# Performance work log

Measured on AMD Instinct MI355X. Metric: run time of the kernel, lower is better.

Reference implementation:

```python
import jax, jax.numpy as jnp
import numpy as np

B, C, W, H = 4, 256, 64, 64
D = C // 8  # reduced query/key channels


def setup_inputs() -> dict:
    key = jax.random.key(0)
    k1, k2, k3, k4, k5 = jax.random.split(key, 5)
    return {
        "x": jax.random.normal(k1, (B, C, W, H), dtype=jnp.float32),
        "q_weight": jax.random.normal(k2, (D, C), dtype=jnp.float32) * 0.05,
        "k_weight": jax.random.normal(k3, (D, C), dtype=jnp.float32) * 0.05,
        "v_weight": jax.random.normal(k4, (C, C), dtype=jnp.float32) * 0.05,
        "gamma": jax.random.normal(k5, (1,), dtype=jnp.float32),
    }


def reference(x, q_weight, k_weight, v_weight, gamma):
    b, c, w, h = x.shape
    n = w * h
    xf = x.reshape(b, c, n)                       # (B, C, N)
    # 1x1 convs == channel matmuls
    q = jnp.einsum('dc,bcn->bdn', q_weight, xf)   # (B, D, N)
    k = jnp.einsum('dc,bcn->bdn', k_weight, xf)   # (B, D, N)
    v = jnp.einsum('oc,bcn->bon', v_weight, xf)   # (B, C, N)
    # energy[b, i, j] = <q[:, i], k[:, j]>  (unscaled, single head)
    energy = jnp.einsum('bdi,bdj->bij', q, k)     # (B, N, N)
    attn = jax.nn.softmax(energy, axis=-1)        # softmax over keys j
    # out[b, c, i] = sum_j v[b, c, j] * attn[b, i, j]
    out = jnp.einsum('bcj,bij->bci', v, attn)     # (B, C, N)
    out = out.reshape(b, c, w, h)
    return gamma[0] * out + x
```

## Files before the change

kernel.cpp:

```cpp
#include <hip/hip_runtime.h>
#include <math.h>

#define Bb 4
#define Cc 256
#define Nn 4096
#define Dd 32
#define XST 264

typedef __attribute__((ext_vector_type(8))) short bf16x8;
typedef __attribute__((ext_vector_type(4))) float f32x4;

__device__ __forceinline__ unsigned short f2bf(float x) {
    union { float f; unsigned u; } c; c.f = x;
    unsigned r = c.u + 0x7fffu + ((c.u >> 16) & 1u);
    return (unsigned short)(r >> 16);
}
__device__ __forceinline__ unsigned pk2(float a, float b) {
    return (unsigned)f2bf(a) | ((unsigned)f2bf(b) << 16);
}
__device__ __forceinline__ float fexp2(float x) {
#if __has_builtin(__builtin_amdgcn_exp2f)
    return __builtin_amdgcn_exp2f(x);
#else
    return __exp2f(x);
#endif
}
__device__ __forceinline__ void wg_barrier() {
    asm volatile("s_waitcnt lgkmcnt(0)\n\ts_barrier" ::: "memory");
}
template <int CTRL>
__device__ __forceinline__ float dppf(float v) {
    int iv = __builtin_bit_cast(int, v);
    return __builtin_bit_cast(float,
        __builtin_amdgcn_update_dpp(iv, iv, CTRL, 0xF, 0xF, false));
}
__device__ __forceinline__ float rowsum16(float v) {
    v += dppf<0xB1>(v);
    v += dppf<0x4E>(v);
    v += dppf<0x141>(v);
    v += dppf<0x140>(v);
    return v;
}

__global__ __launch_bounds__(256) void pack_w(
    const float* __restrict__ qw, const float* __restrict__ kw,
    const float* __restrict__ vw, short* __restrict__ wpk) {
    const int g = blockIdx.x * 256 + threadIdx.x;
    const int qd = g & 3, m = (g >> 2) & 15, kc = (g >> 6) & 7, ot = g >> 9;
    const int o = 16 * ot + m;
    const float* src;
    float scale = 1.0f;
    if (o < 32)      { src = qw + (size_t)o * Cc; scale = 1.44269504088896f; }
    else if (o < 64) { src = kw + (size_t)(o - 32) * Cc; }
    else             { src = vw + (size_t)(o - 64) * Cc; }
    const float* s8 = src + 32 * kc + 8 * qd;
    uint4 u;
    u.x = pk2(s8[0] * scale, s8[1] * scale);
    u.y = pk2(s8[2] * scale, s8[3] * scale);
    u.z = pk2(s8[4] * scale, s8[5] * scale);
    u.w = pk2(s8[6] * scale, s8[7] * scale);
    *(uint4*)(wpk + (size_t)g * 8) = u;
}

__global__ __launch_bounds__(256) void proj(
    const float* __restrict__ x, const short* __restrict__ wpk,
    short* __restrict__ q_t, short* __restrict__ k_t, short* __restrict__ v_b) {
    __shared__ alignas(16) short xs[32 * XST];
    __shared__ alignas(16) short vstage[16384];
    const int b = blockIdx.z;
    const int jt = blockIdx.x;
    const int tid = threadIdx.x;
    const int w = tid >> 6;
    const int lane = tid & 63, qd = lane >> 4, m = lane & 15;

    for (int half = 0; half < 2; ++half) {
        const int n0 = jt * 64 + half * 32;
        if (half) __syncthreads();

        {
            const int n = tid & 31, cg = tid >> 5;
            const float* xp = x + ((size_t)b * Cc + 32 * cg) * Nn + n0 + n;
            float xv[32];
#pragma unroll
            for (int i = 0; i < 32; ++i) xv[i] = xp[(size_t)i * Nn];
            short* row = xs + n * XST + 32 * cg;
#pragma unroll
            for (int u4 = 0; u4 < 4; ++u4)
                *(uint4*)(row + 8 * u4) = make_uint4(
                    pk2(xv[8*u4+0], xv[8*u4+1]), pk2(xv[8*u4+2], xv[8*u4+3]),
                    pk2(xv[8*u4+4], xv[8*u4+5]), pk2(xv[8*u4+6], xv[8*u4+7]));
        }
        __syncthreads();

        const int fslot = m * 4 + qd;
        f32x4 acc[5][2];
#pragma unroll
        for (int i = 0; i < 5; ++i)
#pragma unroll
            for (int nt = 0; nt < 2; ++nt) acc[i][nt] = (f32x4){0.f, 0.f, 0.f, 0.f};

        bf16x8 afc[5], afn[5];
#pragma unroll
        for (int i = 0; i < 5; ++i)
            afc[i] = *(const bf16x8*)(wpk + ((size_t)((4*i + w) * 8 + 0) * 64 + fslot) * 8);

        for (int kc = 0; kc < 8; ++kc) {
            if (kc < 7) {
#pragma unroll
                for (int i = 0; i < 5; ++i)
                    afn[i] = *(const bf16x8*)(
                        wpk + ((size_t)((4*i + w) * 8 + kc + 1) * 64 + fslot) * 8);
            }
            const bf16x8 b0 = *(const bf16x8*)&xs[(     m) * XST + 32 * kc + 8 * qd];
            const bf16x8 b1 = *(const bf16x8*)&xs[(16 + m) * XST + 32 * kc + 8 * qd];
#pragma unroll
            for (int i = 0; i < 5; ++i)
                acc[i][0] = __builtin_amdgcn_mfma_f32_16x16x32_bf16(afc[i], b0, acc[i][0], 0, 0, 0);
#pragma unroll
            for (int i = 0; i < 5; ++i)
                acc[i][1] = __builtin_amdgcn_mfma_f32_16x16x32_bf16(afc[i], b1, acc[i][1], 0, 0, 0);
#pragma unroll
            for (int i = 0; i < 5; ++i) afc[i] = afn[i];
        }

#pragma unroll
        for (int i = 0; i < 5; ++i) {
            const int ot = 4 * i + w;
            if (ot < 4) {
                short* dst = (ot < 2 ? q_t : k_t) + (size_t)b * Nn * Dd;
                const int dbase = (ot & 1) * 16 + 4 * qd;
#pragma unroll
                for (int nt = 0; nt < 2; ++nt) {
                    const f32x4 a = acc[i][nt];
                    *(uint2*)(dst + (size_t)(n0 + 16 * nt + m) * Dd + dbase) =
                        make_uint2(pk2(a[0], a[1]), pk2(a[2], a[3]));
                }
            } else {
                const int ct = ot - 4;
                const int b5 = half;
                const int vbase =
                    ((ct * 2 + (m >> 3)) * 64 + ((m >> 1) & 3) * 16 + 4 * qd) * 8
                    + 4 * (m & 1) + 2 * b5;
#pragma unroll
                for (int rr = 0; rr < 4; ++rr) {
                    const unsigned pv = pk2(acc[i][0][rr], acc[i][1][rr]);
                    *(unsigned*)(vstage + vbase + rr * 8) = pv;
                }
            }
        }
    }
    __syncthreads();

    {
        uint4* dst = (uint4*)(v_b + (size_t)(b * 64 + jt) * 16384);
        const uint4* srcv = (const uint4*)vstage;
#pragma unroll
        for (int i = 0; i < 8; ++i)
            dst[tid + 256 * i] = srcv[tid + 256 * i];
    }
}

__global__ __launch_bounds__(512) void attn(
    const float* __restrict__ x, const short* __restrict__ q_t,
    const short* __restrict__ k_t, const short* __restrict__ v_b,
    const float* __restrict__ gamma, float* __restrict__ out) {
    __shared__ alignas(16) char pool[34304];
    float* l_s = (float*)(pool + 33792);
    float* o_t = (float*)pool;
    short* buf0 = (short*)pool;
    short* buf1 = (short*)(pool + 9216);

    const int fb  = blockIdx.x;
    const int xcd = fb & 7;
    const int b   = xcd >> 1;
    const int i0  = (((xcd & 1) << 5) | (fb >> 3)) << 6;
    const int tid = threadIdx.x;
    const int w = tid >> 6, lane = tid & 63;
    const int qd = lane >> 4, m = lane & 15;
    const int rt = w & 3, kh = w >> 2;

    const bf16x8 af = *(const bf16x8*)(
        q_t + ((size_t)b * Nn + i0 + 16 * rt + m) * Dd + 8 * qd);

    const short* kf = k_t + (size_t)b * Nn * Dd + (32 * kh + m) * Dd + 8 * qd;
    const short* vw = v_b + (size_t)b * (64 * 32 * 64 * 8) + (4 * w) * 512 + lane * 8;

    bf16x8 bkA0 = *(const bf16x8*)(kf);
    bf16x8 bkA1 = *(const bf16x8*)(kf + 512);
    bf16x8 bkB0 = *(const bf16x8*)(kf + 2048);
    bf16x8 bkB1 = *(const bf16x8*)(kf + 2560);
    bf16x8 vfA[2][2], vfB[2][2];
#pragma unroll
    for (int ct = 0; ct < 2; ++ct)
#pragma unroll
        for (int kc = 0; kc < 2; ++kc)
            vfA[ct][kc] = *(const bf16x8*)(vw + (2 * ct + kc) * 512);

    f32x4 oacc[4][2];
#pragma unroll
    for (int mt = 0; mt < 4; ++mt)
#pragma unroll
        for (int ct = 0; ct < 2; ++ct) oacc[mt][ct] = (f32x4){0.f, 0.f, 0.f, 0.f};
    float l_i[4] = {0.f, 0.f, 0.f, 0.f};

    {
        const f32x4 s0 = __builtin_amdgcn_mfma_f32_16x16x32_bf16(
            af, bkA0, (f32x4){0.f, 0.f, 0.f, 0.f}, 0, 0, 0);
        const f32x4 s1 = __builtin_amdgcn_mfma_f32_16x16x32_bf16(
            af, bkA1, (f32x4){0.f, 0.f, 0.f, 0.f}, 0, 0, 0);
        bkA0 = *(const bf16x8*)(kf + 4096);
        bkA1 = *(const bf16x8*)(kf + 4096 + 512);
#pragma unroll
        for (int rr = 0; rr < 4; ++rr) {
            const float p0 = fexp2(s0[rr]);
            const float p1 = fexp2(s1[rr]);
            l_i[rr] += p0 + p1;
            *(unsigned*)&buf0[(16 * rt + 4 * qd + rr) * 72 + 4 * m + 2 * kh] =
                pk2(p0, p1);
        }
        wg_barrier();
    }

    const short* kpre = kf + 3 * 2048;
    const short* vpre = vw + 16384;

    for (int j2 = 0; j2 < 31; ++j2) {
        {
            const f32x4 s0 = __builtin_amdgcn_mfma_f32_16x16x32_bf16(
                af, bkB0, (f32x4){0.f, 0.f, 0.f, 0.f}, 0, 0, 0);
            const f32x4 s1 = __builtin_amdgcn_mfma_f32_16x16x32_bf16(
                af, bkB1, (f32x4){0.f, 0.f, 0.f, 0.f}, 0, 0, 0);
            bkB0 = *(const bf16x8*)(kpre);
            bkB1 = *(const bf16x8*)(kpre + 512);
#pragma unroll
            for (int ct = 0; ct < 2; ++ct)
#pragma unroll
                for (int kc = 0; kc < 2; ++kc)
                    vfB[ct][kc] = *(const bf16x8*)(vpre + (2 * ct + kc) * 512);
            __builtin_amdgcn_s_setprio(1);
#pragma unroll
            for (int kc = 0; kc < 2; ++kc) {
                bf16x8 pa[4];
#pragma unroll
                for (int mt = 0; mt < 4; ++mt)
                    pa[mt] = *(const bf16x8*)&buf0[(16 * mt + m) * 72 + 32 * kc + 8 * qd];
#pragma unroll
                for (int ct = 0; ct < 2; ++ct)
#pragma unroll
                    for (int mt = 0; mt < 4; ++mt)
                        oacc[mt][ct] = __builtin_amdgcn_mfma_f32_16x16x32_bf16(
                            pa[mt], vfA[ct][kc], oacc[mt][ct], 0, 0, 0);
            }
            __builtin_amdgcn_s_setprio(0);
#pragma unroll
            for (int rr = 0; rr < 4; ++rr) {
                const float p0 = fexp2(s0[rr]);
                const float p1 = fexp2(s1[rr]);
                l_i[rr] += p0 + p1;
                *(unsigned*)&buf1[(16 * rt + 4 * qd + rr) * 72 + 4 * m + 2 * kh] =
                    pk2(p0, p1);
            }
            wg_barrier();
        }
        {
            const f32x4 s0 = __builtin_amdgcn_mfma_f32_16x16x32_bf16(
                af, bkA0, (f32x4){0.f, 0.f, 0.f, 0.f}, 0, 0, 0);
            const f32x4 s1 = __builtin_amdgcn_mfma_f32_16x16x32_bf16(
                af, bkA1, (f32x4){0.f, 0.f, 0.f, 0.f}, 0, 0, 0);
            if (j2 < 30) {
                bkA0 = *(const bf16x8*)(kpre + 2048);
                bkA1 = *(const bf16x8*)(kpre + 2560);
            }
#pragma unroll
            for (int ct = 0; ct < 2; ++ct)
#pragma unroll
                for (int kc = 0; kc < 2; ++kc)
                    vfA[ct][kc] = *(const bf16x8*)(vpre + 16384 + (2 * ct + kc) * 512);
            __builtin_amdgcn_s_setprio(1);
#pragma unroll
            for (int kc = 0; kc < 2; ++kc) {
                bf16x8 pa[4];
#pragma unroll
                for (int mt = 0; mt < 4; ++mt)
                    pa[mt] = *(const bf16x8*)&buf1[(16 * mt + m) * 72 + 32 * kc + 8 * qd];
#pragma unroll
                for (int ct = 0; ct < 2; ++ct)
#pragma unroll
                    for (int mt = 0; mt < 4; ++mt)
                        oacc[mt][ct] = __builtin_amdgcn_mfma_f32_16x16x32_bf16(
                            pa[mt], vfB[ct][kc], oacc[mt][ct], 0, 0, 0);
            }
            __builtin_amdgcn_s_setprio(0);
#pragma unroll
            for (int rr = 0; rr < 4; ++rr) {
                const float p0 = fexp2(s0[rr]);
                const float p1 = fexp2(s1[rr]);
                l_i[rr] += p0 + p1;
                *(unsigned*)&buf0[(16 * rt + 4 * qd + rr) * 72 + 4 * m + 2 * kh] =
                    pk2(p0, p1);
            }
            wg_barrier();
        }
        kpre += 4096;
        vpre += 32768;
    }

    {
        const f32x4 s0 = __builtin_amdgcn_mfma_f32_16x16x32_bf16(
            af, bkB0, (f32x4){0.f, 0.f, 0.f, 0.f}, 0, 0, 0);
        const f32x4 s1 = __builtin_amdgcn_mfma_f32_16x16x32_bf16(
            af, bkB1, (f32x4){0.f, 0.f, 0.f, 0.f}, 0, 0, 0);
#pragma unroll
        for (int ct = 0; ct < 2; ++ct)
#pragma unroll
            for (int kc = 0; kc < 2; ++kc)
                vfB[ct][kc] = *(const bf16x8*)(vpre + (2 * ct + kc) * 512);
        __builtin_amdgcn_s_setprio(1);
#pragma unroll
        for (int kc = 0; kc < 2; ++kc) {
            bf16x8 pa[4];
#pragma unroll
            for (int mt = 0; mt < 4; ++mt)
                pa[mt] = *(const bf16x8*)&buf0[(16 * mt + m) * 72 + 32 * kc + 8 * qd];
#pragma unroll
            for (int ct = 0; ct < 2; ++ct)
#pragma unroll
                for (int mt = 0; mt < 4; ++mt)
                    oacc[mt][ct] = __builtin_amdgcn_mfma_f32_16x16x32_bf16(
                        pa[mt], vfA[ct][kc], oacc[mt][ct], 0, 0, 0);
        }
        __builtin_amdgcn_s_setprio(0);
#pragma unroll
        for (int rr = 0; rr < 4; ++rr) {
            const float p0 = fexp2(s0[rr]);
            const float p1 = fexp2(s1[rr]);
            l_i[rr] += p0 + p1;
            *(unsigned*)&buf1[(16 * rt + 4 * qd + rr) * 72 + 4 * m + 2 * kh] =
                pk2(p0, p1);
        }
        wg_barrier();
    }
    {
        __builtin_amdgcn_s_setprio(1);
#pragma unroll
        for (int kc = 0; kc < 2; ++kc) {
            bf16x8 pa[4];
#pragma unroll
            for (int mt = 0; mt < 4; ++mt)
                pa[mt] = *(const bf16x8*)&buf1[(16 * mt + m) * 72 + 32 * kc + 8 * qd];
#pragma unroll
            for (int ct = 0; ct < 2; ++ct)
#pragma unroll
                for (int mt = 0; mt < 4; ++mt)
                    oacc[mt][ct] = __builtin_amdgcn_mfma_f32_16x16x32_bf16(
                        pa[mt], vfB[ct][kc], oacc[mt][ct], 0, 0, 0);
        }
        __builtin_amdgcn_s_setprio(0);
    }

#pragma unroll
    for (int rr = 0; rr < 4; ++rr) l_i[rr] = rowsum16(l_i[rr]);
    if (m == 0)
        *(f32x4*)&l_s[kh * 64 + 16 * rt + 4 * qd] =
            (f32x4){l_i[0], l_i[1], l_i[2], l_i[3]};
    __syncthreads();

    const float g = gamma[0];
    const int i = tid & 63, cg8 = tid >> 6;
    const float linv = 1.0f / (l_s[i] + l_s[64 + i]);
#pragma unroll
    for (int ps = 0; ps < 2; ++ps) {
        if (ps) __syncthreads();
#pragma unroll
        for (int mt = 0; mt < 4; ++mt)
#pragma unroll
            for (int rr = 0; rr < 4; ++rr)
                o_t[(16 * mt + 4 * qd + rr) * 132 + 16 * w + m] = oacc[mt][ps][rr];
        __syncthreads();
#pragma unroll
        for (int u = 0; u < 4; ++u) {
            const f32x4 v4 = *(const f32x4*)&o_t[i * 132 + 16 * cg8 + 4 * u];
#pragma unroll
            for (int e = 0; e < 4; ++e) {
                const int c = 32 * cg8 + 16 * ps + 4 * u + e;
                const size_t gidx = ((size_t)b * Cc + c) * Nn + i0 + i;
                out[gidx] = g * v4[e] * linv + x[gidx];
            }
        }
    }
}

extern "C" void kernel_launch(void* const* d_in, const int* in_sizes, int n_in,
                              void* d_out, int out_size, void* d_ws, size_t ws_size,
                              hipStream_t stream) {
    const float* x     = (const float*)d_in[0];
    const float* qw    = (const float*)d_in[1];
    const float* kw    = (const float*)d_in[2];
    const float* vw    = (const float*)d_in[3];
    const float* gamma = (const float*)d_in[4];
    float* out = (float*)d_out;

    short* q_t = (short*)d_ws;
    short* k_t = q_t + (size_t)Bb * Nn * Dd;
    short* v_b = k_t + (size_t)Bb * Nn * Dd;
    short* wpk = v_b + (size_t)Bb * Cc * Nn;

    pack_w<<<dim3(40), 256, 0, stream>>>(qw, kw, vw, wpk);
    proj<<<dim3(Nn / 64, 1, Bb), 256, 0, stream>>>(x, wpk, q_t, k_t, v_b);
    attn<<<dim3(256), 512, 0, stream>>>(x, q_t, k_t, v_b, gamma, out);
}
```

Before: 133.8 us.

## Split projection kernel across two output-channel groups per 64-column tile

```diff
diff --git a/kernel.cpp b/kernel.cpp
--- a/kernel.cpp
+++ b/kernel.cpp
@@ -62,100 +62,110 @@
     *(uint4*)(wpk + (size_t)g * 8) = u;
 }
 
+template <int NI, int OT0, int CTOFF>
+__device__ __forceinline__ void proj_body(
+    const short* __restrict__ wpk, const short* xs, short* vstage,
+    short* __restrict__ q_t, short* __restrict__ k_t,
+    int b, int n0, int w, int qd, int m) {
+    const int fslot = m * 4 + qd;
+    f32x4 acc[NI][4];
+#pragma unroll
+    for (int i = 0; i < NI; ++i)
+#pragma unroll
+        for (int nt = 0; nt < 4; ++nt) acc[i][nt] = (f32x4){0.f, 0.f, 0.f, 0.f};
+
+    bf16x8 afc[NI], afn[NI];
+#pragma unroll
+    for (int i = 0; i < NI; ++i)
+        afc[i] = *(const bf16x8*)(
+            wpk + ((size_t)((OT0 + 4 * i + w) * 8 + 0) * 64 + fslot) * 8);
+
+    for (int kc = 0; kc < 8; ++kc) {
+        if (kc < 7) {
+#pragma unroll
+            for (int i = 0; i < NI; ++i)
+                afn[i] = *(const bf16x8*)(
+                    wpk + ((size_t)((OT0 + 4 * i + w) * 8 + kc + 1) * 64 + fslot) * 8);
+        }
+        bf16x8 bx[4];
+#pragma unroll
+        for (int nt = 0; nt < 4; ++nt)
+            bx[nt] = *(const bf16x8*)&xs[(16 * nt + m) * XST + 32 * kc + 8 * qd];
+#pragma unroll
+        for (int i = 0; i < NI; ++i)
+#pragma unroll
+            for (int nt = 0; nt < 4; ++nt)
+                acc[i][nt] = __builtin_amdgcn_mfma_f32_16x16x32_bf16(
+                    afc[i], bx[nt], acc[i][nt], 0, 0, 0);
+#pragma unroll
+        for (int i = 0; i < NI; ++i) afc[i] = afn[i];
+    }
+
+#pragma unroll
+    for (int i = 0; i < NI; ++i) {
+        const int ot = OT0 + 4 * i + w;
+        if (ot < 4) {
+            short* dst = (ot < 2 ? q_t : k_t) + (size_t)b * Nn * Dd;
+            const int dbase = (ot & 1) * 16 + 4 * qd;
+#pragma unroll
+            for (int nt = 0; nt < 4; ++nt) {
+                const f32x4 a = acc[i][nt];
+                *(uint2*)(dst + (size_t)(n0 + 16 * nt + m) * Dd + dbase) =
+                    make_uint2(pk2(a[0], a[1]), pk2(a[2], a[3]));
+            }
+        } else {
+            const int gl = (ot - 4 - CTOFF) * 2 + (m >> 3);
+            const int base = (gl * 64 + ((m >> 1) & 3) * 16 + 4 * qd) * 8 + 4 * (m & 1);
+#pragma unroll
+            for (int rr = 0; rr < 4; ++rr)
+                *(uint2*)&vstage[base + rr * 8] = make_uint2(
+                    pk2(acc[i][0][rr], acc[i][1][rr]),
+                    pk2(acc[i][2][rr], acc[i][3][rr]));
+        }
+    }
+}
+
 __global__ __launch_bounds__(256) void proj(
     const float* __restrict__ x, const short* __restrict__ wpk,
     short* __restrict__ q_t, short* __restrict__ k_t, short* __restrict__ v_b) {
-    __shared__ alignas(16) short xs[32 * XST];
-    __shared__ alignas(16) short vstage[16384];
-    const int b = blockIdx.z;
+    __shared__ alignas(16) short xs[64 * XST];
+    __shared__ alignas(16) short vstage[8192];
+    const int b  = blockIdx.z;
+    const int by = blockIdx.y;
     const int jt = blockIdx.x;
+    const int n0 = jt * 64;
     const int tid = threadIdx.x;
     const int w = tid >> 6;
     const int lane = tid & 63, qd = lane >> 4, m = lane & 15;
 
-    for (int half = 0; half < 2; ++half) {
-        const int n0 = jt * 64 + half * 32;
-        if (half) __syncthreads();
-
-        {
-            const int n = tid & 31, cg = tid >> 5;
-            const float* xp = x + ((size_t)b * Cc + 32 * cg) * Nn + n0 + n;
-            float xv[32];
-#pragma unroll
-            for (int i = 0; i < 32; ++i) xv[i] = xp[(size_t)i * Nn];
-            short* row = xs + n * XST + 32 * cg;
-#pragma unroll
-            for (int u4 = 0; u4 < 4; ++u4)
-                *(uint4*)(row + 8 * u4) = make_uint4(
-                    pk2(xv[8*u4+0], xv[8*u4+1]), pk2(xv[8*u4+2], xv[8*u4+3]),
-                    pk2(xv[8*u4+4], xv[8*u4+5]), pk2(xv[8*u4+6], xv[8*u4+7]));
-        }
-        __syncthreads();
-
-        const int fslot = m * 4 + qd;
-        f32x4 acc[5][2];
-#pragma unroll
-        for (int i = 0; i < 5; ++i)
-#pragma unroll
-            for (int nt = 0; nt < 2; ++nt) acc[i][nt] = (f32x4){0.f, 0.f, 0.f, 0.f};
-
-        bf16x8 afc[5], afn[5];
-#pragma unroll
-        for (int i = 0; i < 5; ++i)
-            afc[i] = *(const bf16x8*)(wpk + ((size_t)((4*i + w) * 8 + 0) * 64 + fslot) * 8);
-
-        for (int kc = 0; kc < 8; ++kc) {
-            if (kc < 7) {
-#pragma unroll
-                for (int i = 0; i < 5; ++i)
-                    afn[i] = *(const bf16x8*)(
-                        wpk + ((size_t)((4*i + w) * 8 + kc + 1) * 64 + fslot) * 8);
-            }
-            const bf16x8 b0 = *(const bf16x8*)&xs[(     m) * XST + 32 * kc + 8 * qd];
-            const bf16x8 b1 = *(const bf16x8*)&xs[(16 + m) * XST + 32 * kc + 8 * qd];
-#pragma unroll
-            for (int i = 0; i < 5; ++i)
-                acc[i][0] = __builtin_amdgcn_mfma_f32_16x16x32_bf16(afc[i], b0, acc[i][0], 0, 0, 0);
-#pragma unroll
-            for (int i = 0; i < 5; ++i)
-                acc[i][1] = __builtin_amdgcn_mfma_f32_16x16x32_bf16(afc[i], b1, acc[i][1], 0, 0, 0);
-#pragma unroll
-            for (int i = 0; i < 5; ++i) afc[i] = afn[i];
-        }
-
-#pragma unroll
-        for (int i = 0; i < 5; ++i) {
-            const int ot = 4 * i + w;
-            if (ot < 4) {
-                short* dst = (ot < 2 ? q_t : k_t) + (size_t)b * Nn * Dd;
-                const int dbase = (ot & 1) * 16 + 4 * qd;
-#pragma unroll
-                for (int nt = 0; nt < 2; ++nt) {
-                    const f32x4 a = acc[i][nt];
-                    *(uint2*)(dst + (size_t)(n0 + 16 * nt + m) * Dd + dbase) =
-                        make_uint2(pk2(a[0], a[1]), pk2(a[2], a[3]));
-                }
-            } else {
-                const int ct = ot - 4;
-                const int b5 = half;
-                const int vbase =
-                    ((ct * 2 + (m >> 3)) * 64 + ((m >> 1) & 3) * 16 + 4 * qd) * 8
-                    + 4 * (m & 1) + 2 * b5;
-#pragma unroll
-                for (int rr = 0; rr < 4; ++rr) {
-                    const unsigned pv = pk2(acc[i][0][rr], acc[i][1][rr]);
-                    *(unsigned*)(vstage + vbase + rr * 8) = pv;
-                }
-            }
-        }
+#pragma unroll
+    for (int p = 0; p < 2; ++p) {
+        const int n = tid & 31, cg = tid >> 5;
+        const float* xp = x + ((size_t)b * Cc + 32 * cg) * Nn + n0 + 32 * p + n;
+        float xv[32];
+#pragma unroll
+        for (int i = 0; i < 32; ++i) xv[i] = xp[(size_t)i * Nn];
+        short* row = xs + (32 * p + n) * XST + 32 * cg;
+#pragma unroll
+        for (int u4 = 0; u4 < 4; ++u4)
+            *(uint4*)(row + 8 * u4) = make_uint4(
+                pk2(xv[8*u4+0], xv[8*u4+1]), pk2(xv[8*u4+2], xv[8*u4+3]),
+                pk2(xv[8*u4+4], xv[8*u4+5]), pk2(xv[8*u4+6], xv[8*u4+7]));
     }
     __syncthreads();
 
+    if (by == 0)
+        proj_body<3, 0, 0>(wpk, xs, vstage, q_t, k_t, b, n0, w, qd, m);
+    else
+        proj_body<2, 12, 8>(wpk, xs, vstage, q_t, k_t, b, n0, w, qd, m);
+
+    __syncthreads();
+
     {
-        uint4* dst = (uint4*)(v_b + (size_t)(b * 64 + jt) * 16384);
+        uint4* dst = (uint4*)(v_b + (size_t)(b * 64 + jt) * 16384 + by * 8192);
         const uint4* srcv = (const uint4*)vstage;
 #pragma unroll
-        for (int i = 0; i < 8; ++i)
+        for (int i = 0; i < 4; ++i)
             dst[tid + 256 * i] = srcv[tid + 256 * i];
     }
 }
@@ -406,6 +416,6 @@
     short* wpk = v_b + (size_t)Bb * Cc * Nn;
 
     pack_w<<<dim3(40), 256, 0, stream>>>(qw, kw, vw, wpk);
-    proj<<<dim3(Nn / 64, 1, Bb), 256, 0, stream>>>(x, wpk, q_t, k_t, v_b);
+    proj<<<dim3(Nn / 64, 2, Bb), 256, 0, stream>>>(x, wpk, q_t, k_t, v_b);
     attn<<<dim3(256), 512, 0, stream>>>(x, q_t, k_t, v_b, gamma, out);
 }
```

Measured after the change: 130.5 us. 2.5% less time.
